# Optimization experiments

Measured on AMD Instinct MI355X. Metric: run time of the kernel, lower is better.

The kernel has to match this reference:

```python
import jax, jax.numpy as jnp
import numpy as np

N, R, K = 4, 16384, 96


def setup_inputs() -> dict:
    key = jax.random.key(0)
    k1, k2, k3 = jax.random.split(key, 3)
    rgbs = jax.random.uniform(k1, (N, R, K, 3), dtype=jnp.float32)
    sigmas = jax.random.normal(k2, (N, R, K, 1), dtype=jnp.float32)
    # depths must be monotonically increasing along K (ray sample depths in [0.5, 3.5])
    depths = jnp.sort(0.5 + 3.0 * jax.random.uniform(k3, (N, R, K, 1), dtype=jnp.float32), axis=2)
    return {"rgbs": rgbs, "sigmas": sigmas, "depths": depths}


def reference(rgbs, sigmas, depths):
    # Default rendering_options: use_max_depth=False, no_dist=False,
    # use_mid_point=True, clamp_mode='mipnerf', last_back=False,
    # normalize_rgb=False, normalize_depth=True, clip_depth=True, white_back=False.
    deltas = depths[:, :, 1:] - depths[:, :, :-1]                  # [N,R,K-1,1]
    # midpoint averaging
    rgbs_m = 0.5 * (rgbs[:, :, :-1] + rgbs[:, :, 1:])              # [N,R,K-1,3]
    sigmas_m = 0.5 * (sigmas[:, :, :-1] + sigmas[:, :, 1:])        # [N,R,K-1,1]
    depths_m = 0.5 * (depths[:, :, :-1] + depths[:, :, 1:])        # [N,R,K-1,1]
    # mipnerf clamp: softplus(sigma - 1)
    sig = jax.nn.softplus(sigmas_m - 1.0)
    alphas = 1.0 - jnp.exp(-deltas * sig)                          # [N,R,K-1,1]
    # transmittance via exclusive cumprod along the sample axis
    alphas_shifted = jnp.concatenate(
        [jnp.ones_like(alphas[:, :, :1]), 1.0 - alphas + 1e-10], axis=-2)
    trans = jnp.cumprod(alphas_shifted, axis=-2)[:, :, :-1]        # [N,R,K-1,1]
    weights = alphas * trans                                       # [N,R,K-1,1]
    weights_sum = weights.sum(axis=2)                              # [N,R,1]
    composite_rgb = jnp.sum(weights * rgbs_m, axis=-2)             # [N,R,3]
    composite_depth = jnp.sum(weights * depths_m, axis=-2)         # [N,R,1]
    # normalize_depth=True
    composite_depth = composite_depth / weights_sum
    # clip_depth=True
    composite_depth = jnp.nan_to_num(composite_depth, nan=jnp.inf)
    composite_depth = jnp.clip(composite_depth, depths_m.min(), depths_m.max())
    composite_rgb = composite_rgb * 2.0 - 1.0
    return composite_rgb, composite_depth, weights
```

## Files before the change

kernel.cpp:

```cpp
#include <hip/hip_runtime.h>
#include <math.h>

#define NRAYS     65536
#define RGB_OFF   0
#define DEPTH_OFF (NRAYS * 3)
#define W_OFF     (NRAYS * 4)

#define RPB 16
#define SHD_OFF 0
#define SHS_OFF 1540
#define SHR_OFF 3080
#define SH_TOTAL 7696

typedef float f4u __attribute__((ext_vector_type(4), aligned(4)));
typedef float f2u __attribute__((ext_vector_type(2), aligned(4)));

#define DPPF(oldv, x, ctrl)                                                    \
    __int_as_float(__builtin_amdgcn_update_dpp(                                \
        __float_as_int(oldv), __float_as_int(x), (ctrl), 0xF, 0xF, false))

__device__ __forceinline__ float one_minus_alpha(float x, float delta) {
    const float L2E = 1.44269504088896340736f;
    float xl = x * L2E;
    float l2 = (x > 20.0f) ? xl
                           : __builtin_amdgcn_logf(1.0f + __builtin_amdgcn_exp2f(xl));
    return __builtin_amdgcn_exp2f(-delta * l2);
}

__device__ __forceinline__ void gload_lds16(const float* g, float* l) {
    __builtin_amdgcn_global_load_lds(
        (const __attribute__((address_space(1))) void*)g,
        (__attribute__((address_space(3))) void*)l, 16, 0, 0);
}

__global__ __launch_bounds__(256) void integrate_kernel(
    const float* __restrict__ rgbs,
    const float* __restrict__ sigmas,
    const float* __restrict__ depths,
    float* __restrict__ out)
{
    __shared__ float sh[SH_TOTAL];

    const int t   = threadIdx.x;
    const int w   = t >> 6;
    const int l64 = t & 63;
    const int blk = blockIdx.x;

    {
        const float* gd = depths + (size_t)blk * (RPB * 96);
        const float* gs = sigmas + (size_t)blk * (RPB * 96);
        const float* gr = rgbs   + (size_t)blk * (RPB * 288);
        for (int c = w; c < 30; c += 4) {
            const float* src;
            float* dst;
            if (c < 6)       { src = gd + c * 256;        dst = sh + SHD_OFF + c * 256; }
            else if (c < 12) { src = gs + (c - 6) * 256;  dst = sh + SHS_OFF + (c - 6) * 256; }
            else             { src = gr + (c - 12) * 256; dst = sh + SHR_OFF + (c - 12) * 256; }
            gload_lds16(src + l64 * 4, dst + l64 * 4);
        }
    }
    __builtin_amdgcn_s_waitcnt(0x0F70);
    __syncthreads();

    const int rb_ = t >> 4;
    const int l   = t & 15;
    const int ray = blk * RPB + rb_;
    const bool full = (l < 15);

    const float* db = sh + SHD_OFF + rb_ * 96  + 6 * l;
    const float* sp = sh + SHS_OFF + rb_ * 96  + 6 * l;
    const float* rp = sh + SHR_OFF + rb_ * 288 + 18 * l;

    float2 e0 = *(const float2*)(db);
    float2 e1 = *(const float2*)(db + 2);
    float2 e2 = *(const float2*)(db + 4);
    float2 e3 = *(const float2*)(db + 6);
    float2 f0 = *(const float2*)(sp);
    float2 f1 = *(const float2*)(sp + 2);
    float2 f2v = *(const float2*)(sp + 4);
    float2 f3 = *(const float2*)(sp + 6);
    float2 c0 = *(const float2*)(rp);
    float2 c1 = *(const float2*)(rp + 2);
    float2 c2 = *(const float2*)(rp + 4);
    float2 c3 = *(const float2*)(rp + 6);
    float2 c4 = *(const float2*)(rp + 8);
    float2 c5 = *(const float2*)(rp + 10);
    float2 c6 = *(const float2*)(rp + 12);
    float2 c7 = *(const float2*)(rp + 14);
    float2 c8 = *(const float2*)(rp + 16);
    float2 c9 = *(const float2*)(rp + 18);
    float  r20 = rp[20];

    const float D[7] = {e0.x, e0.y, e1.x, e1.y, e2.x, e2.y, e3.x};
    const float S[7] = {f0.x, f0.y, f1.x, f1.y, f2v.x, f2v.y, f3.x};
    const float R[7] = {c0.x, c1.y, c3.x, c4.y, c6.x, c7.y, c9.x};
    const float G[7] = {c0.y, c2.x, c3.y, c5.x, c6.y, c8.x, c9.y};
    const float B[7] = {c1.x, c2.y, c4.x, c5.y, c7.x, c8.y, r20};

    float u[6];
    float Tloc = 1.0f;
    float Sw = 0.f, Sd = 0.f, Sr = 0.f, Sg = 0.f, Sbv = 0.f;

#define DO_IV(I)                                                      \
    { float delta = D[(I)+1] - D[I];                                  \
      float x = 0.5f * (S[I] + S[(I)+1]) - 1.0f;                      \
      float e = one_minus_alpha(x, delta);                            \
      float uu = (1.0f - e) * Tloc;                                   \
      Tloc *= e + 1e-10f;                                             \
      u[I] = uu;                                                      \
      Sw  += uu;                                                      \
      Sd  += uu * (0.5f * (D[I] + D[(I)+1]));                         \
      Sr  += uu * (0.5f * (R[I] + R[(I)+1]));                         \
      Sg  += uu * (0.5f * (G[I] + G[(I)+1]));                         \
      Sbv += uu * (0.5f * (B[I] + B[(I)+1])); }

    DO_IV(0) DO_IV(1) DO_IV(2) DO_IV(3) DO_IV(4)
    if (full) { DO_IV(5) } else { u[5] = 0.f; }
#undef DO_IV

    float incl = Tloc;
    incl *= DPPF(1.0f, incl, 0x111);
    incl *= DPPF(1.0f, incl, 0x112);
    incl *= DPPF(1.0f, incl, 0x114);
    incl *= DPPF(1.0f, incl, 0x118);
    float Tin = DPPF(1.0f, incl, 0x111);

    Sw *= Tin; Sd *= Tin; Sr *= Tin; Sg *= Tin; Sbv *= Tin;

#define RED(v)                         \
    v += DPPF(0.f, v, 0x111);          \
    v += DPPF(0.f, v, 0x112);          \
    v += DPPF(0.f, v, 0x114);          \
    v += DPPF(0.f, v, 0x118);
    RED(Sw) RED(Sd) RED(Sr) RED(Sg) RED(Sbv)
#undef RED

    float lo0 = 0.5f * (D[0] + D[1]);
    float lo  = DPPF(0.f, lo0, 0x11F);

    float* wout = out + W_OFF + (size_t)ray * 95 + 6 * l;
    f4u v4 = { Tin * u[0], Tin * u[1], Tin * u[2], Tin * u[3] };
    *(f4u*)wout = v4;
    if (full) {
        f2u v2 = { Tin * u[4], Tin * u[5] };
        *(f2u*)(wout + 4) = v2;
    } else {
        wout[4] = Tin * u[4];
    }

    if (l == 15) {
        out[RGB_OFF + ray * 3 + 0] = 2.f * Sr  - 1.f;
        out[RGB_OFF + ray * 3 + 1] = 2.f * Sg  - 1.f;
        out[RGB_OFF + ray * 3 + 2] = 2.f * Sbv - 1.f;
        float dv = Sd / Sw;
        float hi = 0.5f * (D[4] + D[5]);
        dv = fmaxf(fminf(dv, hi), lo);
        out[DEPTH_OFF + ray] = dv;
    }
}

extern "C" void kernel_launch(void* const* d_in, const int* in_sizes, int n_in,
                              void* d_out, int out_size, void* d_ws, size_t ws_size,
                              hipStream_t stream) {
    const float* rgbs   = (const float*)d_in[0];
    const float* sigmas = (const float*)d_in[1];
    const float* depths = (const float*)d_in[2];
    float* out = (float*)d_out;

    integrate_kernel<<<NRAYS / RPB, 256, 0, stream>>>(rgbs, sigmas, depths, out);
}
```

Measured before the change: 157.2 us.

## Make blocks persistent over eight tiles with double-buffered async LDS loads

Each block now processes eight 16-ray tiles in a loop instead of one. It uses two LDS buffers and issues the direct global-to-LDS loads for the next tile before computing the current one, so memory latency overlaps with compute. Partial waitcnt values plus barriers keep the buffers in sync. This cuts the grid size by eight and doubles LDS use per block, which may reduce occupancy and parallelism on a purely bandwidth-bound kernel. The per-wave waitcnt counts depend on how many loads each wave issues, which is fragile.

```diff
diff --git a/kernel.cpp b/kernel.cpp
--- a/kernel.cpp
+++ b/kernel.cpp
@@ -6,11 +6,14 @@
 #define DEPTH_OFF (NRAYS * 3)
 #define W_OFF     (NRAYS * 4)
 
-#define RPB 16
-#define SHD_OFF 0
-#define SHS_OFF 1540
-#define SHR_OFF 3080
-#define SH_TOTAL 7696
+#define RPT  16
+#define TPB  8
+#define NBLK (NRAYS / (RPT * TPB))
+
+#define SHD_OFF   0
+#define SHS_OFF   1540
+#define SHR_OFF   3080
+#define BUF_FLTS  7696
 
 typedef float f4u __attribute__((ext_vector_type(4), aligned(4)));
 typedef float f2u __attribute__((ext_vector_type(2), aligned(4)));
@@ -33,73 +36,87 @@
         (__attribute__((address_space(3))) void*)l, 16, 0, 0);
 }
 
+__device__ __forceinline__ void issue_tile(const float* __restrict__ rgbs,
+                                           const float* __restrict__ sigmas,
+                                           const float* __restrict__ depths,
+                                           int tile, float* buf, int w, int l64) {
+    const float* gd = depths + (size_t)tile * (RPT * 96);
+    const float* gs = sigmas + (size_t)tile * (RPT * 96);
+    const float* gr = rgbs   + (size_t)tile * (RPT * 288);
+    for (int c = w; c < 30; c += 4) {
+        const float* src; float* dst;
+        if (c < 6)       { src = gd + c * 256;        dst = buf + SHD_OFF + c * 256; }
+        else if (c < 12) { src = gs + (c - 6) * 256;  dst = buf + SHS_OFF + (c - 6) * 256; }
+        else             { src = gr + (c - 12) * 256; dst = buf + SHR_OFF + (c - 12) * 256; }
+        gload_lds16(src + l64 * 4, dst + l64 * 4);
+    }
+}
+
 __global__ __launch_bounds__(256) void integrate_kernel(
     const float* __restrict__ rgbs,
     const float* __restrict__ sigmas,
     const float* __restrict__ depths,
     float* __restrict__ out)
 {
-    __shared__ float sh[SH_TOTAL];
+    __shared__ float sh[2 * BUF_FLTS];
 
-    const int t   = threadIdx.x;
-    const int w   = t >> 6;
-    const int l64 = t & 63;
-    const int blk = blockIdx.x;
+    const int t    = threadIdx.x;
+    const int w    = t >> 6;
+    const int l64  = t & 63;
+    const int rb_  = t >> 4;
+    const int l    = t & 15;
+    const bool full = (l < 15);
+    const int tile0 = blockIdx.x * TPB;
 
-    {
-        const float* gd = depths + (size_t)blk * (RPB * 96);
-        const float* gs = sigmas + (size_t)blk * (RPB * 96);
-        const float* gr = rgbs   + (size_t)blk * (RPB * 288);
-        for (int c = w; c < 30; c += 4) {
-            const float* src;
-            float* dst;
-            if (c < 6)       { src = gd + c * 256;        dst = sh + SHD_OFF + c * 256; }
-            else if (c < 12) { src = gs + (c - 6) * 256;  dst = sh + SHS_OFF + (c - 6) * 256; }
-            else             { src = gr + (c - 12) * 256; dst = sh + SHR_OFF + (c - 12) * 256; }
-            gload_lds16(src + l64 * 4, dst + l64 * 4);
+    issue_tile(rgbs, sigmas, depths, tile0, sh, w, l64);
+
+    for (int i = 0; i < TPB; ++i) {
+        float* buf = sh + (i & 1) * BUF_FLTS;
+
+        if (i + 1 < TPB) {
+            issue_tile(rgbs, sigmas, depths, tile0 + i + 1,
+                       sh + ((i + 1) & 1) * BUF_FLTS, w, l64);
+            if (w < 2) __builtin_amdgcn_s_waitcnt(0x0F78);
+            else       __builtin_amdgcn_s_waitcnt(0x0F77);
+        } else {
+            __builtin_amdgcn_s_waitcnt(0x0F70);
         }
-    }
-    __builtin_amdgcn_s_waitcnt(0x0F70);
-    __syncthreads();
+        __builtin_amdgcn_s_barrier();
 
-    const int rb_ = t >> 4;
-    const int l   = t & 15;
-    const int ray = blk * RPB + rb_;
-    const bool full = (l < 15);
+        const int ray = (tile0 + i) * RPT + rb_;
+        const float* db = buf + SHD_OFF + rb_ * 96  + 6 * l;
+        const float* sp = buf + SHS_OFF + rb_ * 96  + 6 * l;
+        const float* rp = buf + SHR_OFF + rb_ * 288 + 18 * l;
 
-    const float* db = sh + SHD_OFF + rb_ * 96  + 6 * l;
-    const float* sp = sh + SHS_OFF + rb_ * 96  + 6 * l;
-    const float* rp = sh + SHR_OFF + rb_ * 288 + 18 * l;
+        float2 e0 = *(const float2*)(db);
+        float2 e1 = *(const float2*)(db + 2);
+        float2 e2 = *(const float2*)(db + 4);
+        float2 e3 = *(const float2*)(db + 6);
+        float2 f0 = *(const float2*)(sp);
+        float2 f1 = *(const float2*)(sp + 2);
+        float2 f2v = *(const float2*)(sp + 4);
+        float2 f3 = *(const float2*)(sp + 6);
+        float2 c0 = *(const float2*)(rp);
+        float2 c1 = *(const float2*)(rp + 2);
+        float2 c2 = *(const float2*)(rp + 4);
+        float2 c3 = *(const float2*)(rp + 6);
+        float2 c4 = *(const float2*)(rp + 8);
+        float2 c5 = *(const float2*)(rp + 10);
+        float2 c6 = *(const float2*)(rp + 12);
+        float2 c7 = *(const float2*)(rp + 14);
+        float2 c8 = *(const float2*)(rp + 16);
+        float2 c9 = *(const float2*)(rp + 18);
+        float  r20 = rp[20];
 
-    float2 e0 = *(const float2*)(db);
-    float2 e1 = *(const float2*)(db + 2);
-    float2 e2 = *(const float2*)(db + 4);
-    float2 e3 = *(const float2*)(db + 6);
-    float2 f0 = *(const float2*)(sp);
-    float2 f1 = *(const float2*)(sp + 2);
-    float2 f2v = *(const float2*)(sp + 4);
-    float2 f3 = *(const float2*)(sp + 6);
-    float2 c0 = *(const float2*)(rp);
-    float2 c1 = *(const float2*)(rp + 2);
-    float2 c2 = *(const float2*)(rp + 4);
-    float2 c3 = *(const float2*)(rp + 6);
-    float2 c4 = *(const float2*)(rp + 8);
-    float2 c5 = *(const float2*)(rp + 10);
-    float2 c6 = *(const float2*)(rp + 12);
-    float2 c7 = *(const float2*)(rp + 14);
-    float2 c8 = *(const float2*)(rp + 16);
-    float2 c9 = *(const float2*)(rp + 18);
-    float  r20 = rp[20];
+        const float D[7] = {e0.x, e0.y, e1.x, e1.y, e2.x, e2.y, e3.x};
+        const float S[7] = {f0.x, f0.y, f1.x, f1.y, f2v.x, f2v.y, f3.x};
+        const float R[7] = {c0.x, c1.y, c3.x, c4.y, c6.x, c7.y, c9.x};
+        const float G[7] = {c0.y, c2.x, c3.y, c5.x, c6.y, c8.x, c9.y};
+        const float B[7] = {c1.x, c2.y, c4.x, c5.y, c7.x, c8.y, r20};
 
-    const float D[7] = {e0.x, e0.y, e1.x, e1.y, e2.x, e2.y, e3.x};
-    const float S[7] = {f0.x, f0.y, f1.x, f1.y, f2v.x, f2v.y, f3.x};
-    const float R[7] = {c0.x, c1.y, c3.x, c4.y, c6.x, c7.y, c9.x};
-    const float G[7] = {c0.y, c2.x, c3.y, c5.x, c6.y, c8.x, c9.y};
-    const float B[7] = {c1.x, c2.y, c4.x, c5.y, c7.x, c8.y, r20};
-
-    float u[6];
-    float Tloc = 1.0f;
-    float Sw = 0.f, Sd = 0.f, Sr = 0.f, Sg = 0.f, Sbv = 0.f;
+        float u[6];
+        float Tloc = 1.0f;
+        float Sw = 0.f, Sd = 0.f, Sr = 0.f, Sg = 0.f, Sbv = 0.f;
 
 #define DO_IV(I)                                                      \
     { float delta = D[(I)+1] - D[I];                                  \
@@ -114,48 +131,51 @@
       Sg  += uu * (0.5f * (G[I] + G[(I)+1]));                         \
       Sbv += uu * (0.5f * (B[I] + B[(I)+1])); }
 
-    DO_IV(0) DO_IV(1) DO_IV(2) DO_IV(3) DO_IV(4)
-    if (full) { DO_IV(5) } else { u[5] = 0.f; }
+        DO_IV(0) DO_IV(1) DO_IV(2) DO_IV(3) DO_IV(4)
+        if (full) { DO_IV(5) } else { u[5] = 0.f; }
 #undef DO_IV
 
-    float incl = Tloc;
-    incl *= DPPF(1.0f, incl, 0x111);
-    incl *= DPPF(1.0f, incl, 0x112);
-    incl *= DPPF(1.0f, incl, 0x114);
-    incl *= DPPF(1.0f, incl, 0x118);
-    float Tin = DPPF(1.0f, incl, 0x111);
+        float incl = Tloc;
+        incl *= DPPF(1.0f, incl, 0x111);
+        incl *= DPPF(1.0f, incl, 0x112);
+        incl *= DPPF(1.0f, incl, 0x114);
+        incl *= DPPF(1.0f, incl, 0x118);
+        float Tin = DPPF(1.0f, incl, 0x111);
 
-    Sw *= Tin; Sd *= Tin; Sr *= Tin; Sg *= Tin; Sbv *= Tin;
+        Sw *= Tin; Sd *= Tin; Sr *= Tin; Sg *= Tin; Sbv *= Tin;
 
 #define RED(v)                         \
-    v += DPPF(0.f, v, 0x111);          \
-    v += DPPF(0.f, v, 0x112);          \
-    v += DPPF(0.f, v, 0x114);          \
-    v += DPPF(0.f, v, 0x118);
-    RED(Sw) RED(Sd) RED(Sr) RED(Sg) RED(Sbv)
+        v += DPPF(0.f, v, 0x111);      \
+        v += DPPF(0.f, v, 0x112);      \
+        v += DPPF(0.f, v, 0x114);      \
+        v += DPPF(0.f, v, 0x118);
+        RED(Sw) RED(Sd) RED(Sr) RED(Sg) RED(Sbv)
 #undef RED
 
-    float lo0 = 0.5f * (D[0] + D[1]);
-    float lo  = DPPF(0.f, lo0, 0x11F);
+        float lo0 = 0.5f * (D[0] + D[1]);
+        float lo  = DPPF(0.f, lo0, 0x11F);
 
-    float* wout = out + W_OFF + (size_t)ray * 95 + 6 * l;
-    f4u v4 = { Tin * u[0], Tin * u[1], Tin * u[2], Tin * u[3] };
-    *(f4u*)wout = v4;
-    if (full) {
-        f2u v2 = { Tin * u[4], Tin * u[5] };
-        *(f2u*)(wout + 4) = v2;
-    } else {
-        wout[4] = Tin * u[4];
-    }
+        float* wout = out + W_OFF + (size_t)ray * 95 + 6 * l;
+        f4u v4 = { Tin * u[0], Tin * u[1], Tin * u[2], Tin * u[3] };
+        *(f4u*)wout = v4;
+        if (full) {
+            f2u v2 = { Tin * u[4], Tin * u[5] };
+            *(f2u*)(wout + 4) = v2;
+        } else {
+            wout[4] = Tin * u[4];
+        }
 
-    if (l == 15) {
-        out[RGB_OFF + ray * 3 + 0] = 2.f * Sr  - 1.f;
-        out[RGB_OFF + ray * 3 + 1] = 2.f * Sg  - 1.f;
-        out[RGB_OFF + ray * 3 + 2] = 2.f * Sbv - 1.f;
-        float dv = Sd / Sw;
-        float hi = 0.5f * (D[4] + D[5]);
-        dv = fmaxf(fminf(dv, hi), lo);
-        out[DEPTH_OFF + ray] = dv;
+        if (l == 15) {
+            out[RGB_OFF + ray * 3 + 0] = 2.f * Sr  - 1.f;
+            out[RGB_OFF + ray * 3 + 1] = 2.f * Sg  - 1.f;
+            out[RGB_OFF + ray * 3 + 2] = 2.f * Sbv - 1.f;
+            float dv = Sd / Sw;
+            float hi = 0.5f * (D[4] + D[5]);
+            dv = fmaxf(fminf(dv, hi), lo);
+            out[DEPTH_OFF + ray] = dv;
+        }
+
+        __builtin_amdgcn_s_barrier();
     }
 }
 
@@ -167,5 +187,5 @@
     const float* depths = (const float*)d_in[2];
     float* out = (float*)d_out;
 
-    integrate_kernel<<<NRAYS / RPB, 256, 0, stream>>>(rgbs, sigmas, depths, out);
+    integrate_kernel<<<NBLK, 256, 0, stream>>>(rgbs, sigmas, depths, out);
 }
```

Result: slower. 163.3 us (+3.9%).
